# Optimization experiments

Hardware: AMD Instinct MI355X
Metric: run time of the kernel (lower is better)

## Reference

```python
import jax, jax.numpy as jnp
import numpy as np

T, B, D, H = 1024, 256, 256, 256


def setup_inputs() -> dict:
    key = jax.random.key(0)
    k1, k2, k3, k4 = jax.random.split(key, 4)
    ins = jax.random.normal(k1, (T, B, D), dtype=jnp.float32)
    resets = jax.random.randint(k2, (T, B), 0, 2).astype(jnp.bool_)
    init_h = jnp.zeros((B, H), dtype=jnp.float32)
    # packed GRU weights in (r, z, n) order; flax GRUCell: input dense has no
    # bias, hidden dense has bias, and r gates (Wh_n @ h + b_n).
    Wi = jax.random.normal(k3, (D, 3 * H), dtype=jnp.float32) / np.sqrt(D)
    Wh = jax.random.normal(k4, (H, 3 * H), dtype=jnp.float32) / np.sqrt(H)
    b = jnp.zeros((3 * H,), dtype=jnp.float32)
    return {"ins": ins, "resets": resets, "init_h": init_h,
            "Wi": Wi, "Wh": Wh, "b": b}


def reference(ins, resets, init_h, Wi, Wh, b):
    def step(h, xt):
        x, reset = xt                                  # x: [B,D], reset: [B]
        h = jnp.where(reset[:, None], jnp.zeros_like(h), h)
        gi = x @ Wi                                    # [B,3H] (no input bias)
        gh = h @ Wh + b                                # [B,3H] (hidden bias)
        ir, iz, i_n = jnp.split(gi, 3, axis=-1)
        hr, hz, h_n = jnp.split(gh, 3, axis=-1)
        r = jax.nn.sigmoid(ir + hr)
        z = jax.nn.sigmoid(iz + hz)
        n = jnp.tanh(i_n + r * h_n)                    # r gates (Wh_n h + b_n)
        new_h = (1.0 - z) * n + z * h
        return new_h, new_h                            # GRU: y == new hidden

    h_final, ys = jax.lax.scan(step, init_h, (ins, resets))
    return ys                                          # [T,B,H]
```

## Files before the change

kernel.cpp:

```cpp
#include <hip/hip_runtime.h>


typedef __attribute__((ext_vector_type(8))) short sv8;
typedef __attribute__((ext_vector_type(4))) short sv4;
typedef __attribute__((ext_vector_type(4))) float fv4;

#define HPAD 264

static __device__ __forceinline__ unsigned short f2bf(float f) {
  unsigned int u = __float_as_uint(f);
  u += 0x7fffu + ((u >> 16) & 1u);
  return (unsigned short)(u >> 16);
}
static __device__ __forceinline__ float bf2f(unsigned short s) {
  return __uint_as_float(((unsigned int)s) << 16);
}

static __device__ __forceinline__ void gload16(const void* g, void* l) {
  __builtin_amdgcn_global_load_lds((__attribute__((address_space(1))) void*)g,
                                   (__attribute__((address_space(3))) void*)l,
                                   16, 0, 0);
}

__global__ __launch_bounds__(256) void transpose_w(
    const float* __restrict__ Wi, const float* __restrict__ Wh,
    unsigned short* __restrict__ Wt, unsigned short* __restrict__ Wht) {
  __shared__ float tile[32][33];
  const int bid = blockIdx.x;
  const float* src = (bid < 192) ? Wi : Wh;
  unsigned short* dst = (bid < 192) ? Wt : Wht;
  const int local = bid % 192;
  const int c0 = (local % 24) * 32;
  const int k0 = (local / 24) * 32;
  const int t = threadIdx.x, tr = t >> 5, tc = t & 31;
#pragma unroll
  for (int p = 0; p < 4; ++p) {
    int k = tr + p * 8;
    tile[k][tc] = src[(size_t)(k0 + k) * 768 + c0 + tc];
  }
  __syncthreads();
#pragma unroll
  for (int p = 0; p < 4; ++p) {
    int c = tr + p * 8;
    dst[(size_t)(c0 + c) * 256 + k0 + tc] = f2bf(tile[tc][c]);
  }
}

__global__ __launch_bounds__(256) void conv_bf16(
    const float* __restrict__ src, unsigned short* __restrict__ dst, int n8) {
  int i = blockIdx.x * 256 + threadIdx.x;
  const int stride = gridDim.x * 256;
  for (; i < n8; i += stride) {
    fv4 a = *(const fv4*)(src + (size_t)i * 8);
    fv4 b = *(const fv4*)(src + (size_t)i * 8 + 4);
    sv8 o = {(short)f2bf(a[0]), (short)f2bf(a[1]), (short)f2bf(a[2]), (short)f2bf(a[3]),
             (short)f2bf(b[0]), (short)f2bf(b[1]), (short)f2bf(b[2]), (short)f2bf(b[3])};
    *(sv8*)(dst + (size_t)i * 8) = o;
  }
}

__global__ __launch_bounds__(256) void gi_gemm2(
    const unsigned short* __restrict__ insb,
    const unsigned short* __restrict__ Wt,
    unsigned short* __restrict__ gi, int w0) {
  __shared__ __align__(16) unsigned short As[4096];
  __shared__ __align__(16) unsigned short Bs[4096];
  const int t = threadIdx.x;
  const int wave = t >> 6, lane = t & 63;
  const int n16 = lane & 15, quad = lane >> 4;
  const int n0 = blockIdx.x * 128;
  const int m0 = blockIdx.y * 128;
  const int m0w = (wave & 1) * 64, n0w = (wave >> 1) * 64;

  const int c0i = wave * 128 + lane;
  const int c1i = c0i + 64;
  const int r0 = ((c0i >> 5) << 3) | (c0i & 7), k0c = ((c0i >> 3) & 3) * 8;
  const int r1 = ((c1i >> 5) << 3) | (c1i & 7), k1c = ((c1i >> 3) & 3) * 8;
  unsigned short* ldA0 = As + (size_t)(wave * 2) * 512;
  unsigned short* ldA1 = As + (size_t)(wave * 2 + 1) * 512;
  unsigned short* ldB0 = Bs + (size_t)(wave * 2) * 512;
  unsigned short* ldB1 = Bs + (size_t)(wave * 2 + 1) * 512;
  const unsigned short* gA0 = insb + (size_t)(w0 * 256 + m0 + r0) * 256 + k0c;
  const unsigned short* gA1 = insb + (size_t)(w0 * 256 + m0 + r1) * 256 + k1c;
  const unsigned short* gB0 = Wt + (size_t)(n0 + r0) * 256 + k0c;
  const unsigned short* gB1 = Wt + (size_t)(n0 + r1) * 256 + k1c;

  const int arow = m0w + n16, brow = n0w + n16;
  const char* apb = (const char*)As + ((arow >> 3) << 9) + (quad << 7) + ((arow & 7) << 4);
  const char* bpb = (const char*)Bs + ((brow >> 3) << 9) + (quad << 7) + ((brow & 7) << 4);

  fv4 acc[4][4] = {};
  for (int kb = 0; kb < 8; ++kb) {
    gload16(gA0 + kb * 32, ldA0);
    gload16(gA1 + kb * 32, ldA1);
    gload16(gB0 + kb * 32, ldB0);
    gload16(gB1 + kb * 32, ldB1);
    __syncthreads();
    sv8 af[4], bfr[4];
#pragma unroll
    for (int mt = 0; mt < 4; ++mt) af[mt] = *(const sv8*)(apb + mt * 1024);
#pragma unroll
    for (int nt = 0; nt < 4; ++nt) bfr[nt] = *(const sv8*)(bpb + nt * 1024);
#pragma unroll
    for (int mt = 0; mt < 4; ++mt)
#pragma unroll
      for (int nt = 0; nt < 4; ++nt)
        acc[mt][nt] = __builtin_amdgcn_mfma_f32_16x16x32_bf16(af[mt], bfr[nt], acc[mt][nt], 0, 0, 0);
    __syncthreads();
  }
#pragma unroll
  for (int mt = 0; mt < 4; ++mt)
#pragma unroll
    for (int i = 0; i < 4; ++i) {
      const int row = m0 + m0w + mt * 16 + quad * 4 + i;
      unsigned short* gp = gi + (size_t)row * 768 + n0 + n0w + n16;
#pragma unroll
      for (int nt = 0; nt < 4; ++nt) gp[nt * 16] = f2bf(acc[mt][nt][i]);
    }
}

__global__ __launch_bounds__(512, 2) void rec_kernel(
    const unsigned short* __restrict__ gi,
    const int* __restrict__ resets,
    const float* __restrict__ h_in,
    float* __restrict__ h_carry,
    const unsigned short* __restrict__ Wht,
    const float* __restrict__ bias,
    float* __restrict__ out,
    int t0, int wsteps) {
  __shared__ __align__(16) unsigned short whn[256][HPAD];
  __shared__ __align__(16) unsigned short hbuf[2][16][HPAD];
  __shared__ int rstl[1024];
  __shared__ int cand[16];
  __shared__ int cstart[17];
  __shared__ int s_smax;

  const int tid = threadIdx.x;
  const int wave = tid >> 6, lane = tid & 63;
  const int n16 = lane & 15, quad = lane >> 4;
  const int b = blockIdx.x;
  const int wcb = wave * 16;

  for (int e = tid; e < 8192; e += 512) {
    const int col = e >> 5, kc = (e & 31) * 8;
    *(sv8*)&whn[col][kc] = *(const sv8*)(Wht + (size_t)(512 + col) * 256 + kc);
  }
  for (int e = tid; e < wsteps; e += 512)
    rstl[e] = resets[(size_t)(t0 + e) * 256 + b];
  if (tid < 16) cand[tid] = wsteps;
  __syncthreads();

  {
    int span = wsteps >> 4;
    if (span < 1) span = 1;
    for (int e = tid; e < wsteps; e += 512)
      if (rstl[e]) {
        const int j = e / span;
        if (j < 16) atomicMin(&cand[j], e);
      }
  }
  {
    const int row = tid >> 5, c8 = (tid & 31) * 8;
    sv8 pk = {0, 0, 0, 0, 0, 0, 0, 0};
    if (row == 0 && !rstl[0]) {
      fv4 v0 = *(const fv4*)(h_in + (size_t)b * 256 + c8);
      fv4 v1 = *(const fv4*)(h_in + (size_t)b * 256 + c8 + 4);
#pragma unroll
      for (int j = 0; j < 4; ++j) pk[j] = (short)f2bf(v0[j]);
#pragma unroll
      for (int j = 0; j < 4; ++j) pk[4 + j] = (short)f2bf(v1[j]);
    }
    *(sv8*)&hbuf[0][row][c8] = pk;
  }
  __syncthreads();
  if (tid == 0) {
    int S[17];
    S[16] = wsteps;
    for (int j = 15; j >= 0; --j) S[j] = (cand[j] < wsteps) ? cand[j] : S[j + 1];
    int cnt = 1;
    cstart[0] = 0;
    for (int r = 1; r < 16; ++r) {
      const int v = S[r];
      if (v < wsteps && v > cstart[cnt - 1]) cstart[cnt++] = v;
    }
    for (int r = cnt; r <= 16; ++r) cstart[r] = wsteps;
    int mx = 0;
    for (int r = 0; r < 16; ++r) {
      const int L = cstart[r + 1] - cstart[r];
      if (L > mx) mx = L;
    }
    s_smax = mx;
  }
  __syncthreads();

  int rs_[4], rl_[4];
#pragma unroll
  for (int i = 0; i < 4; ++i) {
    const int ri = quad * 4 + i;
    rs_[i] = cstart[ri];
    rl_[i] = cstart[ri + 1] - rs_[i];
  }
  float hprev[4][2];
#pragma unroll
  for (int i = 0; i < 4; ++i)
#pragma unroll
    for (int c = 0; c < 2; ++c)
      hprev[i][c] = (rs_[i] == 0) ? h_in[(size_t)b * 256 + c * 128 + wcb + n16] : 0.f;

  sv8 whf[2][2][8];
#pragma unroll
  for (int g = 0; g < 2; ++g)
#pragma unroll
    for (int c = 0; c < 2; ++c)
#pragma unroll
      for (int kt = 0; kt < 8; ++kt)
        whf[g][c][kt] = *(const sv8*)(Wht + (size_t)(g * 256 + c * 128 + wcb + n16) * 256 + kt * 32 + quad * 8);

  float b_r[2], b_z[2], b_n[2];
#pragma unroll
  for (int c = 0; c < 2; ++c) {
    const int col = c * 128 + wcb + n16;
    b_r[c] = bias[col];
    b_z[c] = bias[256 + col];
    b_n[c] = bias[512 + col];
  }

  const size_t boff = (size_t)b * 768 + wcb + n16;
  const unsigned short* pmax = gi + (size_t)(wsteps - 1) * 196608 + boff;
  const unsigned short* gp[4];
#pragma unroll
  for (int i = 0; i < 4; ++i) {
    const int r0 = (rs_[i] < wsteps) ? rs_[i] : (wsteps - 1);
    gp[i] = gi + (size_t)r0 * 196608 + boff;
  }
  float* ob0 = out + (size_t)t0 * 65536 + (size_t)b * 256 + wcb + n16;
  const int smax = s_smax;

  unsigned short A_[2][3][4], B_[2][3][4];
#pragma unroll
  for (int i = 0; i < 4; ++i)
#pragma unroll
    for (int c = 0; c < 2; ++c) {
      A_[c][0][i] = gp[i][c * 128];
      A_[c][1][i] = gp[i][c * 128 + 256];
      A_[c][2][i] = gp[i][c * 128 + 512];
    }
  int rc[4];
#pragma unroll
  for (int i = 0; i < 4; ++i) rc[i] = (rl_[i] > 0) ? rstl[rs_[i]] : 1;

  auto step = [&](int s, unsigned short (&cur)[2][3][4], unsigned short (&nxt)[2][3][4]) {
    const int rb = s & 1, wb = rb ^ 1;
    fv4 acc[3][2] = {};
#pragma unroll
    for (int kt = 0; kt < 8; ++kt) {
      sv8 hf = *(const sv8*)&hbuf[rb][n16][kt * 32 + quad * 8];
#pragma unroll
      for (int c = 0; c < 2; ++c) {
        sv8 wnf = *(const sv8*)&whn[c * 128 + wcb + n16][kt * 32 + quad * 8];
        acc[0][c] = __builtin_amdgcn_mfma_f32_16x16x32_bf16(hf, whf[0][c][kt], acc[0][c], 0, 0, 0);
        acc[1][c] = __builtin_amdgcn_mfma_f32_16x16x32_bf16(hf, whf[1][c][kt], acc[1][c], 0, 0, 0);
        acc[2][c] = __builtin_amdgcn_mfma_f32_16x16x32_bf16(hf, wnf, acc[2][c], 0, 0, 0);
      }
    }
#pragma unroll
    for (int i = 0; i < 4; ++i) {
      gp[i] += 196608;
      if (gp[i] > pmax) gp[i] = pmax;
#pragma unroll
      for (int c = 0; c < 2; ++c) {
        nxt[c][0][i] = gp[i][c * 128];
        nxt[c][1][i] = gp[i][c * 128 + 256];
        nxt[c][2][i] = gp[i][c * 128 + 512];
      }
    }
    int nf[4], lt[4];
    bool act[4];
    float hnew[4][2];
#pragma unroll
    for (int i = 0; i < 4; ++i) {
      lt[i] = rs_[i] + s;
      act[i] = (s < rl_[i]);
      nf[i] = (s + 1 < rl_[i]) ? rstl[lt[i] + 1] : 1;
#pragma unroll
      for (int c = 0; c < 2; ++c) {
        const float pre_r = bf2f(cur[c][0][i]) + acc[0][c][i] + b_r[c];
        const float pre_z = bf2f(cur[c][1][i]) + acc[1][c][i] + b_z[c];
        const float r = __builtin_amdgcn_rcpf(1.f + __expf(-pre_r));
        const float z = __builtin_amdgcn_rcpf(1.f + __expf(-pre_z));
        const float npre = bf2f(cur[c][2][i]) + r * (acc[2][c][i] + b_n[c]);
        const float n = 1.f - 2.f * __builtin_amdgcn_rcpf(1.f + __expf(2.f * npre));
        const float hp = rc[i] ? 0.f : hprev[i][c];
        const float h = (1.f - z) * n + z * hp;
        hnew[i][c] = h;
        hprev[i][c] = h;
        hbuf[wb][quad * 4 + i][c * 128 + wcb + n16] = nf[i] ? (unsigned short)0 : f2bf(h);
      }
    }
    __builtin_amdgcn_sched_barrier(0);
    asm volatile("s_waitcnt lgkmcnt(0)" ::: "memory");
    __builtin_amdgcn_s_barrier();
    __builtin_amdgcn_sched_barrier(0);
#pragma unroll
    for (int i = 0; i < 4; ++i) {
      if (act[i]) {
#pragma unroll
        for (int c = 0; c < 2; ++c) {
          ob0[(size_t)lt[i] * 65536 + c * 128] = hnew[i][c];
          if (lt[i] == wsteps - 1)
            h_carry[(size_t)b * 256 + c * 128 + wcb + n16] = hnew[i][c];
        }
      }
      rc[i] = nf[i];
    }
  };

  for (int s = 0; s < smax; s += 2) {
    step(s, A_, B_);
    if (s + 1 < smax) step(s + 1, B_, A_);
  }
}

extern "C" void kernel_launch(void* const* d_in, const int* in_sizes, int n_in,
                              void* d_out, int out_size, void* d_ws, size_t ws_size,
                              hipStream_t stream) {
  const float* ins    = (const float*)d_in[0];
  const int* resets   = (const int*)d_in[1];
  const float* init_h = (const float*)d_in[2];
  const float* Wi     = (const float*)d_in[3];
  const float* Wh     = (const float*)d_in[4];
  const float* bias   = (const float*)d_in[5];
  float* out          = (float*)d_out;

  char* ws = (char*)d_ws;
  unsigned short* Wt   = (unsigned short*)ws;
  unsigned short* Wht  = (unsigned short*)(ws + 393216);
  float* h_carry       = (float*)(ws + 786432);
  unsigned short* insb = (unsigned short*)(ws + 1048576);
  const size_t gi_off  = 1048576 + 134217728;
  unsigned short* gi   = (unsigned short*)(ws + gi_off);

  int wsteps = 1024;
  while (wsteps > 2 && gi_off + (size_t)wsteps * 256 * 768 * 2 > ws_size) wsteps >>= 1;
  const int nwin = 1024 / wsteps;

  hipLaunchKernelGGL(transpose_w, dim3(384), dim3(256), 0, stream, Wi, Wh, Wt, Wht);
  hipLaunchKernelGGL(conv_bf16, dim3(2048), dim3(256), 0, stream, ins, insb, 8388608);
  for (int w = 0; w < nwin; ++w) {
    const int t0 = w * wsteps;
    hipLaunchKernelGGL(gi_gemm2, dim3(6, wsteps * 2), dim3(256), 0, stream, insb, Wt, gi, t0);
    hipLaunchKernelGGL(rec_kernel, dim3(256), dim3(512), 0, stream,
                       gi, resets, (w == 0 ? init_h : h_carry), h_carry, Wht, bias, out, t0, wsteps);
  }
}
```

Measured before the change: 931.7 us.

## Keep full A row-tile resident in LDS and loop over all N tiles per block

The input-projection GEMM now loads a 128x256 tile of the bf16 inputs into LDS once per block and iterates over all six 128-wide output column tiles, streaming only the weight tiles. Before, each block reloaded its A slice for every N tile, so the inputs were read six times from global memory. The cost is 64KB of LDS per block, a 6x smaller grid, and weight loads that are not double-buffered and sit between two barriers per k-step.

```diff
diff --git a/kernel.cpp b/kernel.cpp
--- a/kernel.cpp
+++ b/kernel.cpp
@@ -59,64 +59,79 @@
   }
 }
 
-__global__ __launch_bounds__(256) void gi_gemm2(
+__global__ __launch_bounds__(256, 2) void gi_gemm3(
     const unsigned short* __restrict__ insb,
     const unsigned short* __restrict__ Wt,
     unsigned short* __restrict__ gi, int w0) {
-  __shared__ __align__(16) unsigned short As[4096];
+  __shared__ __align__(16) unsigned short As[32768];
   __shared__ __align__(16) unsigned short Bs[4096];
   const int t = threadIdx.x;
   const int wave = t >> 6, lane = t & 63;
   const int n16 = lane & 15, quad = lane >> 4;
-  const int n0 = blockIdx.x * 128;
-  const int m0 = blockIdx.y * 128;
+  const int m0 = blockIdx.x * 128;
   const int m0w = (wave & 1) * 64, n0w = (wave >> 1) * 64;
 
   const int c0i = wave * 128 + lane;
   const int c1i = c0i + 64;
   const int r0 = ((c0i >> 5) << 3) | (c0i & 7), k0c = ((c0i >> 3) & 3) * 8;
   const int r1 = ((c1i >> 5) << 3) | (c1i & 7), k1c = ((c1i >> 3) & 3) * 8;
-  unsigned short* ldA0 = As + (size_t)(wave * 2) * 512;
-  unsigned short* ldA1 = As + (size_t)(wave * 2 + 1) * 512;
-  unsigned short* ldB0 = Bs + (size_t)(wave * 2) * 512;
-  unsigned short* ldB1 = Bs + (size_t)(wave * 2 + 1) * 512;
-  const unsigned short* gA0 = insb + (size_t)(w0 * 256 + m0 + r0) * 256 + k0c;
-  const unsigned short* gA1 = insb + (size_t)(w0 * 256 + m0 + r1) * 256 + k1c;
-  const unsigned short* gB0 = Wt + (size_t)(n0 + r0) * 256 + k0c;
-  const unsigned short* gB1 = Wt + (size_t)(n0 + r1) * 256 + k1c;
+
+  {
+    const unsigned short* gA0 = insb + (size_t)(w0 * 256 + m0 + r0) * 256 + k0c;
+    const unsigned short* gA1 = insb + (size_t)(w0 * 256 + m0 + r1) * 256 + k1c;
+    unsigned short* dA0 = As + wave * 1024;
+    unsigned short* dA1 = dA0 + 512;
+#pragma unroll
+    for (int kb = 0; kb < 8; ++kb) {
+      gload16(gA0 + kb * 32, dA0 + kb * 4096);
+      gload16(gA1 + kb * 32, dA1 + kb * 4096);
+    }
+  }
+  const unsigned short* gB0 = Wt + (size_t)r0 * 256 + k0c;
+  const unsigned short* gB1 = Wt + (size_t)r1 * 256 + k1c;
+  unsigned short* dB0 = Bs + wave * 1024;
+  unsigned short* dB1 = dB0 + 512;
+  gload16(gB0, dB0);
+  gload16(gB1, dB1);
+  __syncthreads();
 
   const int arow = m0w + n16, brow = n0w + n16;
   const char* apb = (const char*)As + ((arow >> 3) << 9) + (quad << 7) + ((arow & 7) << 4);
   const char* bpb = (const char*)Bs + ((brow >> 3) << 9) + (quad << 7) + ((brow & 7) << 4);
 
-  fv4 acc[4][4] = {};
-  for (int kb = 0; kb < 8; ++kb) {
-    gload16(gA0 + kb * 32, ldA0);
-    gload16(gA1 + kb * 32, ldA1);
-    gload16(gB0 + kb * 32, ldB0);
-    gload16(gB1 + kb * 32, ldB1);
-    __syncthreads();
-    sv8 af[4], bfr[4];
-#pragma unroll
-    for (int mt = 0; mt < 4; ++mt) af[mt] = *(const sv8*)(apb + mt * 1024);
-#pragma unroll
-    for (int nt = 0; nt < 4; ++nt) bfr[nt] = *(const sv8*)(bpb + nt * 1024);
+  for (int nt = 0; nt < 6; ++nt) {
+    fv4 acc[4][4] = {};
+#pragma unroll
+    for (int kb = 0; kb < 8; ++kb) {
+      sv8 af[4], bfr[4];
+#pragma unroll
+      for (int mt = 0; mt < 4; ++mt) af[mt] = *(const sv8*)(apb + kb * 8192 + mt * 1024);
+#pragma unroll
+      for (int j = 0; j < 4; ++j) bfr[j] = *(const sv8*)(bpb + j * 1024);
+#pragma unroll
+      for (int mt = 0; mt < 4; ++mt)
+#pragma unroll
+        for (int j = 0; j < 4; ++j)
+          acc[mt][j] = __builtin_amdgcn_mfma_f32_16x16x32_bf16(af[mt], bfr[j], acc[mt][j], 0, 0, 0);
+      __syncthreads();
+      const int step = nt * 8 + kb + 1;
+      if (step < 48) {
+        const int nn = step >> 3, nk = step & 7;
+        gload16(gB0 + (size_t)nn * 32768 + nk * 32, dB0);
+        gload16(gB1 + (size_t)nn * 32768 + nk * 32, dB1);
+      }
+      __syncthreads();
+    }
 #pragma unroll
     for (int mt = 0; mt < 4; ++mt)
 #pragma unroll
-      for (int nt = 0; nt < 4; ++nt)
-        acc[mt][nt] = __builtin_amdgcn_mfma_f32_16x16x32_bf16(af[mt], bfr[nt], acc[mt][nt], 0, 0, 0);
-    __syncthreads();
-  }
-#pragma unroll
-  for (int mt = 0; mt < 4; ++mt)
-#pragma unroll
-    for (int i = 0; i < 4; ++i) {
-      const int row = m0 + m0w + mt * 16 + quad * 4 + i;
-      unsigned short* gp = gi + (size_t)row * 768 + n0 + n0w + n16;
-#pragma unroll
-      for (int nt = 0; nt < 4; ++nt) gp[nt * 16] = f2bf(acc[mt][nt][i]);
-    }
+      for (int i = 0; i < 4; ++i) {
+        const int row = m0 + m0w + mt * 16 + quad * 4 + i;
+        unsigned short* gp = gi + (size_t)row * 768 + nt * 128 + n0w + n16;
+#pragma unroll
+        for (int j = 0; j < 4; ++j) gp[j * 16] = f2bf(acc[mt][j][i]);
+      }
+  }
 }
 
 __global__ __launch_bounds__(512, 2) void rec_kernel(
@@ -348,7 +363,7 @@
   hipLaunchKernelGGL(conv_bf16, dim3(2048), dim3(256), 0, stream, ins, insb, 8388608);
   for (int w = 0; w < nwin; ++w) {
     const int t0 = w * wsteps;
-    hipLaunchKernelGGL(gi_gemm2, dim3(6, wsteps * 2), dim3(256), 0, stream, insb, Wt, gi, t0);
+    hipLaunchKernelGGL(gi_gemm3, dim3(wsteps * 2), dim3(256), 0, stream, insb, Wt, gi, t0);
     hipLaunchKernelGGL(rec_kernel, dim3(256), dim3(512), 0, stream,
                        gi, resets, (w == 0 ? init_h : h_carry), h_carry, Wht, bias, out, t0, wsteps);
   }
```

Result: faster. 858.5 us (-7.9%).
